# Kernel optimization log

Hardware: AMD Instinct MI355X
Metric: run time of the kernel (lower is better)

Reference implementation:

```python
import jax, jax.numpy as jnp
import numpy as np
from jax import lax

B, TIN, N, M, O, LM, TDEC = 64, 128, 256, 1024, 512, 2048, 64
LN_EPS = 1e-5


def setup_inputs() -> dict:
    key = jax.random.key(0)
    ks = jax.random.split(key, 32)
    s = 0.02
    p = lambda k, shape: (jax.random.normal(k, shape, jnp.float32) * s)
    z = lambda n: jnp.zeros((n,), jnp.float32)
    return {
        "X": jax.random.normal(ks[0], (B, TIN, N), jnp.float32),
        "Y0": jax.random.uniform(ks[1], (B, 1, O), jnp.float32),
        # encoder GRU, 2 layers (PyTorch layout: W_ih [3m,in], W_hh [3m,m])
        "enc_Wih0": p(ks[2], (3 * M, N)), "enc_Whh0": p(ks[3], (3 * M, M)),
        "enc_bih0": z(3 * M), "enc_bhh0": z(3 * M),
        "enc_Wih1": p(ks[4], (3 * M, M)), "enc_Whh1": p(ks[5], (3 * M, M)),
        "enc_bih1": z(3 * M), "enc_bhh1": z(3 * M),
        # decoder GRU, 2 layers (layer0 input dim = O)
        "dec_Wih0": p(ks[6], (3 * M, O)), "dec_Whh0": p(ks[7], (3 * M, M)),
        "dec_bih0": z(3 * M), "dec_bhh0": z(3 * M),
        "dec_Wih1": p(ks[8], (3 * M, M)), "dec_Whh1": p(ks[9], (3 * M, M)),
        "dec_bih1": z(3 * M), "dec_bhh1": z(3 * M),
        # decoder head
        "fc1_w": p(ks[10], (LM, M)), "fc1_b": z(LM),
        "ln_g": jnp.ones((LM,), jnp.float32), "ln_b": z(LM),
        "fc2_w": p(ks[11], (O, LM)), "fc2_b": z(O),
    }


def _gru_step(h, x, Wih, Whh, bih, bhh):
    # PyTorch GRU cell: gates ordered (r, z, n)
    gi = x @ Wih.T + bih          # [B, 3m]
    gh = h @ Whh.T + bhh          # [B, 3m]
    i_r, i_z, i_n = jnp.split(gi, 3, axis=-1)
    h_r, h_z, h_n = jnp.split(gh, 3, axis=-1)
    r = jax.nn.sigmoid(i_r + h_r)
    zg = jax.nn.sigmoid(i_z + h_z)
    n = jnp.tanh(i_n + r * h_n)
    return (1.0 - zg) * n + zg * h


def reference(X, Y0,
              enc_Wih0, enc_Whh0, enc_bih0, enc_bhh0,
              enc_Wih1, enc_Whh1, enc_bih1, enc_bhh1,
              dec_Wih0, dec_Whh0, dec_bih0, dec_bhh0,
              dec_Wih1, dec_Whh1, dec_bih1, dec_bhh1,
              fc1_w, fc1_b, ln_g, ln_b, fc2_w, fc2_b):
    batch = X.shape[0]
    # ---- encoder: 2-layer GRU over time ----
    seq = jnp.swapaxes(X, 0, 1)  # [T, B, n]
    enc_layers = [(enc_Wih0, enc_Whh0, enc_bih0, enc_bhh0),
                  (enc_Wih1, enc_Whh1, enc_bih1, enc_bhh1)]
    h_final = []
    for (Wih, Whh, bih, bhh) in enc_layers:
        def f(h, x, Wih=Wih, Whh=Whh, bih=bih, bhh=bhh):
            hn = _gru_step(h, x, Wih, Whh, bih, bhh)
            return hn, hn
        hT, seq = lax.scan(f, jnp.zeros((batch, M), X.dtype), seq)
        h_final.append(hT)

    dec0 = (dec_Wih0, dec_Whh0, dec_bih0, dec_bhh0)
    dec1 = (dec_Wih1, dec_Whh1, dec_bih1, dec_bhh1)
    y_init = Y0[:, 0, :]  # [B, o]

    def step(carry, _):
        h0, h1, y = carry
        h0n = _gru_step(h0, y, *dec0)
        h1n = _gru_step(h1, h0n, *dec1)
        z = h1n @ fc1_w.T + fc1_b                      # [B, l_m]
        mu = jnp.mean(z, axis=-1, keepdims=True)
        var = jnp.var(z, axis=-1, keepdims=True)
        z = (z - mu) * lax.rsqrt(var + LN_EPS) * ln_g + ln_b
        z = jax.nn.gelu(z, approximate=False)
        out = z @ fc2_w.T + fc2_b                      # [B, o]
        yn = jax.nn.softmax(out, axis=-1)
        return (h0n, h1n, yn), out

    _, outs = lax.scan(step, (h_final[0], h_final[1], y_init), None, length=TDEC)
    return jnp.swapaxes(outs, 0, 1)  # [B, TDEC, o]
```

## Files before the change

kernel.cpp:

```cpp
#include <hip/hip_runtime.h>
#include <math.h>

#define B 64
#define TIN 128
#define N_IN 256
#define M 1024
#define O_DIM 512
#define LM 2048
#define TDEC 64
#define M3 3072
#define CH 8
#define NB 256

typedef short bf16x8 __attribute__((ext_vector_type(8)));
typedef float floatx4 __attribute__((ext_vector_type(4)));
typedef unsigned long long u64_t;

__device__ __forceinline__ unsigned short f2bf(float f) {
    unsigned int u = __float_as_uint(f);
    u += 0x7FFFu + ((u >> 16) & 1u);
    return (unsigned short)(u >> 16);
}
__device__ __forceinline__ float sigm(float x) { return 1.f / (1.f + expf(-x)); }

__device__ __forceinline__ float ald_f(const float* p) {
    return __hip_atomic_load((float*)p, __ATOMIC_RELAXED, __HIP_MEMORY_SCOPE_AGENT);
}
__device__ __forceinline__ void ast_f(float* p, float v) {
    __hip_atomic_store(p, v, __ATOMIC_RELAXED, __HIP_MEMORY_SCOPE_AGENT);
}
__device__ __forceinline__ void ast_u(unsigned* p, unsigned v) {
    __hip_atomic_store(p, v, __ATOMIC_RELAXED, __HIP_MEMORY_SCOPE_AGENT);
}
__device__ __forceinline__ bf16x8 ald_b8(const short* p) {
    u64_t lo = __hip_atomic_load((u64_t*)p, __ATOMIC_RELAXED, __HIP_MEMORY_SCOPE_AGENT);
    u64_t hi = __hip_atomic_load((u64_t*)(p + 4), __ATOMIC_RELAXED, __HIP_MEMORY_SCOPE_AGENT);
    union { u64_t q[2]; bf16x8 v; } u;
    u.q[0] = lo; u.q[1] = hi;
    return u.v;
}
__device__ __forceinline__ void ast_h_pair(short* addr_even, float hv) {
    unsigned short hb16 = f2bf(hv);
    int partner = __shfl_xor((int)hb16, 1, 64);
    if ((threadIdx.x & 1) == 0) {
        unsigned pair = (unsigned)hb16 | ((unsigned)(unsigned short)partner << 16);
        __hip_atomic_store((unsigned*)addr_even, pair,
                           __ATOMIC_RELAXED, __HIP_MEMORY_SCOPE_AGENT);
    }
}

__device__ __forceinline__ void gridbar(unsigned* flags, unsigned epoch, int bid) {
    __syncthreads();
    if (threadIdx.x == 0)
        __hip_atomic_store(&flags[(size_t)bid * 32], epoch, __ATOMIC_RELAXED,
                           __HIP_MEMORY_SCOPE_AGENT);
    unsigned g = 0;
    while (__hip_atomic_load(&flags[(size_t)threadIdx.x * 32],
                             __ATOMIC_RELAXED, __HIP_MEMORY_SCOPE_AGENT) < epoch) {
        __builtin_amdgcn_s_sleep(2);
        if (++g > (1u << 22)) break;
    }
    __syncthreads();
}

__global__ __launch_bounds__(256) void cast_bf(const float* __restrict__ in,
                                               short* __restrict__ out, int n) {
    int i = blockIdx.x * 256 + threadIdx.x;
    if (i < n) out[i] = (short)f2bf(in[i]);
}

__global__ __launch_bounds__(256) void transpose_X_bf(const float* __restrict__ X,
                                                      short* __restrict__ Xt) {
    int idx = blockIdx.x * 256 + threadIdx.x;
    int n = idx & (N_IN - 1);
    int b = (idx >> 8) & (B - 1);
    int t = idx >> 14;
    Xt[idx] = (short)f2bf(X[(b * TIN + t) * N_IN + n]);
}

struct EncArgs {
    const short* Xt;
    short* seqA;
    float* gi;
    const short* wih0; const short* whh0; const float* bih0; const float* bhh0;
    const short* wih1; const short* whh1; const float* bih1; const float* bhh1;
    float* h0f; float* h1f;
    short* h0b; short* h1b;
    unsigned* flags;
};

__global__ __launch_bounds__(256, 1) void enc_mega(EncArgs a) {
    __shared__ float lds[3][4][64][4];
    const int bid  = blockIdx.x;
    const int wave = threadIdx.x >> 6;
    const int lane = threadIdx.x & 63;
    const int lrow = lane & 15;
    const int ko8  = (lane >> 4) * 8;
    unsigned epoch = 0;

    for (int layer = 0; layer < 2; ++layer) {
        const short* Wih = layer ? a.wih1 : a.wih0;
        const short* Whh = layer ? a.whh1 : a.whh0;
        const float* bih = layer ? a.bih1 : a.bih0;
        const float* bhh = layer ? a.bhh1 : a.bhh0;
        const short* inseq = layer ? a.seqA : a.Xt;
        const int K = layer ? M : N_IN;
        float* hf = layer ? a.h1f : a.h0f;
        short* hb = layer ? a.h1b : a.h0b;

        for (int c = 0; c < TIN / CH; ++c) {
            {
                const short* A = inseq + (size_t)c * CH * B * K;
                int xcd = bid & 7;
                int l   = bid >> 3;
                int w4  = l * 4 + wave;
                for (int i = 0; i < 6; ++i) {
                    int gt   = w4 * 6 + i;
                    int colt = xcd * 24 + (gt % 24);
                    int rowt = gt / 24;
                    int r0 = rowt * 16;
                    int c0 = colt * 16;
                    const short* ap = A + (size_t)(r0 + lrow) * K + ko8;
                    const short* wp = Wih + (size_t)(c0 + lrow) * K + ko8;
                    floatx4 acc = {0.f, 0.f, 0.f, 0.f};
                    #pragma unroll 4
                    for (int k = 0; k < K; k += 32) {
                        bf16x8 av = *(const bf16x8*)(ap + k);
                        bf16x8 bv = *(const bf16x8*)(wp + k);
                        acc = __builtin_amdgcn_mfma_f32_16x16x32_bf16(av, bv, acc, 0, 0, 0);
                    }
                    int col = c0 + lrow;
                    float bv = bih[col];
                    int rb = r0 + (lane >> 4) * 4;
                    #pragma unroll
                    for (int q = 0; q < 4; q++)
                        ast_f(&a.gi[(size_t)(rb + q) * M3 + col], acc[q] + bv);
                }
            }
            gridbar(a.flags, ++epoch, bid);
            for (int tt = 0; tt < CH; ++tt) {
                int t = c * CH + tt;
                int pin = t & 1, pout = pin ^ 1;
                const short* h_in = hb + (size_t)pin * B * M;
                float* gi_t = a.gi + (size_t)tt * B * M3;
                int m0 = (bid & 63) * 16;
                int r0 = (bid >> 6) * 16;
                const int Kq = M >> 2;
                const short* ap = h_in + (size_t)(r0 + lrow) * M + wave * Kq + ko8;
                bf16x8 hreg[8];
                #pragma unroll
                for (int k = 0; k < 8; ++k) hreg[k] = ald_b8(ap + k * 32);
                const short* wr = Whh + (size_t)(m0 + lrow) * M + wave * Kq + ko8;
                const short* wz = wr + (size_t)M * M;
                const short* wn = wr + (size_t)2 * M * M;
                floatx4 ar = {0.f, 0.f, 0.f, 0.f};
                floatx4 az = {0.f, 0.f, 0.f, 0.f};
                floatx4 ah = {0.f, 0.f, 0.f, 0.f};
                #pragma unroll
                for (int k = 0; k < 8; ++k) {
                    ar = __builtin_amdgcn_mfma_f32_16x16x32_bf16(hreg[k], *(const bf16x8*)(wr + k * 32), ar, 0, 0, 0);
                    az = __builtin_amdgcn_mfma_f32_16x16x32_bf16(hreg[k], *(const bf16x8*)(wz + k * 32), az, 0, 0, 0);
                    ah = __builtin_amdgcn_mfma_f32_16x16x32_bf16(hreg[k], *(const bf16x8*)(wn + k * 32), ah, 0, 0, 0);
                }
                #pragma unroll
                for (int i = 0; i < 4; i++) {
                    lds[0][wave][lane][i] = ar[i];
                    lds[1][wave][lane][i] = az[i];
                    lds[2][wave][lane][i] = ah[i];
                }
                __syncthreads();
                int row = threadIdx.x >> 4, col = threadIdx.x & 15;
                int sl = (row >> 2) * 16 + col, rg = row & 3;
                float sr = lds[0][0][sl][rg] + lds[0][1][sl][rg] + lds[0][2][sl][rg] + lds[0][3][sl][rg];
                float sz = lds[1][0][sl][rg] + lds[1][1][sl][rg] + lds[1][2][sl][rg] + lds[1][3][sl][rg];
                float sn = lds[2][0][sl][rg] + lds[2][1][sl][rg] + lds[2][2][sl][rg] + lds[2][3][sl][rg];
                int b = r0 + row, m = m0 + col;
                float gr = ald_f(&gi_t[(size_t)b * M3 + m]);
                float gz = ald_f(&gi_t[(size_t)b * M3 + M + m]);
                float gn = ald_f(&gi_t[(size_t)b * M3 + 2 * M + m]);
                float r = sigm(gr + sr + bhh[m]);
                float z = sigm(gz + sz + bhh[M + m]);
                float n = tanhf(gn + r * (sn + bhh[2 * M + m]));
                size_t hi = (size_t)b * M + m;
                float hv = (1.f - z) * n + z * hf[hi];
                hf[hi] = hv;
                if (layer == 0) a.seqA[(size_t)t * B * M + hi] = (short)f2bf(hv);
                ast_h_pair(hb + (size_t)pout * B * M + (size_t)b * M + (m & ~1),
                           hv);
                gridbar(a.flags, ++epoch, bid);
            }
        }
        if (layer == 0) {
            __builtin_amdgcn_fence(__ATOMIC_RELEASE, "agent");
            gridbar(a.flags, ++epoch, bid);
            __builtin_amdgcn_fence(__ATOMIC_ACQUIRE, "agent");
        }
    }
}

struct DecArgs {
    const short* yb;
    const short* wih0; const short* whh0; const float* bih0; const float* bhh0;
    const short* wih1; const short* whh1; const float* bih1; const float* bhh1;
    const short* wfc1; const float* fc1b;
    const float* lng; const float* lnb;
    const short* wfc2; const float* fc2b;
    float* h0f; float* h1f;
    short* h0b; short* h1b;
    float* zb;
    short* zbb;
    float* part;
    float* out;
    unsigned* flags;
};

__global__ __launch_bounds__(256, 1) void dec_mega(DecArgs a) {
    __shared__ short xs[16 * O_DIM];
    __shared__ float lds[4][4][64][4];
    __shared__ float redD[2];
    const int bid  = blockIdx.x;
    const int wave = threadIdx.x >> 6;
    const int lane = threadIdx.x & 63;
    const int lrow = lane & 15;
    const int ko8  = (lane >> 4) * 8;
    const int ldl  = TDEC * O_DIM;
    unsigned epoch = 0;

    for (int t = 0; t < TDEC; ++t) {
        int pin = t & 1, pout = pin ^ 1;
        int m0 = (bid & 63) * 16;
        int r0 = (bid >> 6) * 16;
        {
            const int KqH = M >> 2;
            const short* apH = a.h0b + (size_t)pin * B * M + (size_t)(r0 + lrow) * M + wave * KqH + ko8;
            bf16x8 hreg[8];
            #pragma unroll
            for (int k = 0; k < 8; ++k) hreg[k] = ald_b8(apH + k * 32);

            int rr = wave * 4 + (lane >> 4);
            int cl = lane & 15;
            if (t > 0) {
                const float* rowp = a.out + (size_t)(r0 + rr) * ldl
                                  + (size_t)(t - 1) * O_DIM + cl * 32;
                float v[32];
                float mx = -3.4e38f;
                #pragma unroll
                for (int j = 0; j < 32; j++) { v[j] = ald_f(rowp + j); mx = fmaxf(mx, v[j]); }
                #pragma unroll
                for (int off = 1; off < 16; off <<= 1) mx = fmaxf(mx, __shfl_xor(mx, off, 16));
                float s = 0.f;
                #pragma unroll
                for (int j = 0; j < 32; j++) { v[j] = __expf(v[j] - mx); s += v[j]; }
                #pragma unroll
                for (int off = 1; off < 16; off <<= 1) s += __shfl_xor(s, off, 16);
                float inv = 1.f / s;
                #pragma unroll
                for (int j = 0; j < 32; j += 2) {
                    unsigned int pk = (unsigned int)f2bf(v[j] * inv)
                                    | ((unsigned int)f2bf(v[j + 1] * inv) << 16);
                    int byte = ((rr * O_DIM + cl * 32 + j) * 2) ^ ((rr & 7) << 4);
                    *(unsigned int*)((char*)xs + byte) = pk;
                }
            } else {
                const short* rowp = a.yb + (size_t)(r0 + rr) * O_DIM + cl * 32;
                #pragma unroll
                for (int j = 0; j < 32; j += 2) {
                    unsigned int pk = (unsigned int)(unsigned short)rowp[j]
                                    | ((unsigned int)(unsigned short)rowp[j + 1] << 16);
                    int byte = ((rr * O_DIM + cl * 32 + j) * 2) ^ ((rr & 7) << 4);
                    *(unsigned int*)((char*)xs + byte) = pk;
                }
            }
            __syncthreads();
            const int KqI = O_DIM >> 2;
            const short* wrI = a.wih0 + (size_t)(m0 + lrow) * O_DIM + wave * KqI + ko8;
            const short* wzI = wrI + (size_t)M * O_DIM;
            const short* wnI = wrI + (size_t)2 * M * O_DIM;
            const short* wrH = a.whh0 + (size_t)(m0 + lrow) * M + wave * KqH + ko8;
            const short* wzH = wrH + (size_t)M * M;
            const short* wnH = wrH + (size_t)2 * M * M;
            floatx4 ar = {0.f, 0.f, 0.f, 0.f};
            floatx4 az = {0.f, 0.f, 0.f, 0.f};
            floatx4 ai = {0.f, 0.f, 0.f, 0.f};
            floatx4 ah = {0.f, 0.f, 0.f, 0.f};
            #pragma unroll
            for (int k = 0; k < KqI; k += 32) {
                int abyte = ((lrow * O_DIM + wave * KqI + ko8 + k) * 2) ^ ((lrow & 7) << 4);
                bf16x8 av = *(const bf16x8*)((const char*)xs + abyte);
                ar = __builtin_amdgcn_mfma_f32_16x16x32_bf16(av, *(const bf16x8*)(wrI + k), ar, 0, 0, 0);
                az = __builtin_amdgcn_mfma_f32_16x16x32_bf16(av, *(const bf16x8*)(wzI + k), az, 0, 0, 0);
                ai = __builtin_amdgcn_mfma_f32_16x16x32_bf16(av, *(const bf16x8*)(wnI + k), ai, 0, 0, 0);
            }
            #pragma unroll
            for (int k = 0; k < 8; ++k) {
                ar = __builtin_amdgcn_mfma_f32_16x16x32_bf16(hreg[k], *(const bf16x8*)(wrH + k * 32), ar, 0, 0, 0);
                az = __builtin_amdgcn_mfma_f32_16x16x32_bf16(hreg[k], *(const bf16x8*)(wzH + k * 32), az, 0, 0, 0);
                ah = __builtin_amdgcn_mfma_f32_16x16x32_bf16(hreg[k], *(const bf16x8*)(wnH + k * 32), ah, 0, 0, 0);
            }
            #pragma unroll
            for (int i = 0; i < 4; i++) {
                lds[0][wave][lane][i] = ar[i];
                lds[1][wave][lane][i] = az[i];
                lds[2][wave][lane][i] = ai[i];
                lds[3][wave][lane][i] = ah[i];
            }
            __syncthreads();
            int row = threadIdx.x >> 4, col = threadIdx.x & 15;
            int sl = (row >> 2) * 16 + col, rg = row & 3;
            float sr = lds[0][0][sl][rg] + lds[0][1][sl][rg] + lds[0][2][sl][rg] + lds[0][3][sl][rg];
            float sz = lds[1][0][sl][rg] + lds[1][1][sl][rg] + lds[1][2][sl][rg] + lds[1][3][sl][rg];
            float si = lds[2][0][sl][rg] + lds[2][1][sl][rg] + lds[2][2][sl][rg] + lds[2][3][sl][rg];
            float sh = lds[3][0][sl][rg] + lds[3][1][sl][rg] + lds[3][2][sl][rg] + lds[3][3][sl][rg];
            int b = r0 + row, m = m0 + col;
            float r = sigm(sr + a.bih0[m] + a.bhh0[m]);
            float z = sigm(sz + a.bih0[M + m] + a.bhh0[M + m]);
            float n = tanhf(si + a.bih0[2 * M + m] + r * (sh + a.bhh0[2 * M + m]));
            size_t hi = (size_t)b * M + m;
            float hv = (1.f - z) * n + z * a.h0f[hi];
            a.h0f[hi] = hv;
            ast_h_pair(a.h0b + (size_t)pout * B * M + (size_t)b * M + (m & ~1), hv);
        }
        gridbar(a.flags, ++epoch, bid);
        {
            const int Kq = M >> 2;
            const short* apI = a.h0b + (size_t)pout * B * M + (size_t)(r0 + lrow) * M + wave * Kq + ko8;
            const short* apH = a.h1b + (size_t)pin * B * M + (size_t)(r0 + lrow) * M + wave * Kq + ko8;
            bf16x8 ireg[8], hreg[8];
            #pragma unroll
            for (int k = 0; k < 8; ++k) ireg[k] = ald_b8(apI + k * 32);
            #pragma unroll
            for (int k = 0; k < 8; ++k) hreg[k] = ald_b8(apH + k * 32);
            const short* wrI = a.wih1 + (size_t)(m0 + lrow) * M + wave * Kq + ko8;
            const short* wzI = wrI + (size_t)M * M;
            const short* wnI = wrI + (size_t)2 * M * M;
            const short* wrH = a.whh1 + (size_t)(m0 + lrow) * M + wave * Kq + ko8;
            const short* wzH = wrH + (size_t)M * M;
            const short* wnH = wrH + (size_t)2 * M * M;
            floatx4 ar = {0.f, 0.f, 0.f, 0.f};
            floatx4 az = {0.f, 0.f, 0.f, 0.f};
            floatx4 ai = {0.f, 0.f, 0.f, 0.f};
            floatx4 ah = {0.f, 0.f, 0.f, 0.f};
            #pragma unroll
            for (int k = 0; k < 8; ++k) {
                ar = __builtin_amdgcn_mfma_f32_16x16x32_bf16(ireg[k], *(const bf16x8*)(wrI + k * 32), ar, 0, 0, 0);
                az = __builtin_amdgcn_mfma_f32_16x16x32_bf16(ireg[k], *(const bf16x8*)(wzI + k * 32), az, 0, 0, 0);
                ai = __builtin_amdgcn_mfma_f32_16x16x32_bf16(ireg[k], *(const bf16x8*)(wnI + k * 32), ai, 0, 0, 0);
            }
            #pragma unroll
            for (int k = 0; k < 8; ++k) {
                ar = __builtin_amdgcn_mfma_f32_16x16x32_bf16(hreg[k], *(const bf16x8*)(wrH + k * 32), ar, 0, 0, 0);
                az = __builtin_amdgcn_mfma_f32_16x16x32_bf16(hreg[k], *(const bf16x8*)(wzH + k * 32), az, 0, 0, 0);
                ah = __builtin_amdgcn_mfma_f32_16x16x32_bf16(hreg[k], *(const bf16x8*)(wnH + k * 32), ah, 0, 0, 0);
            }
            #pragma unroll
            for (int i = 0; i < 4; i++) {
                lds[0][wave][lane][i] = ar[i];
                lds[1][wave][lane][i] = az[i];
                lds[2][wave][lane][i] = ai[i];
                lds[3][wave][lane][i] = ah[i];
            }
            __syncthreads();
            int row = threadIdx.x >> 4, col = threadIdx.x & 15;
            int sl = (row >> 2) * 16 + col, rg = row & 3;
            float sr = lds[0][0][sl][rg] + lds[0][1][sl][rg] + lds[0][2][sl][rg] + lds[0][3][sl][rg];
            float sz = lds[1][0][sl][rg] + lds[1][1][sl][rg] + lds[1][2][sl][rg] + lds[1][3][sl][rg];
            float si = lds[2][0][sl][rg] + lds[2][1][sl][rg] + lds[2][2][sl][rg] + lds[2][3][sl][rg];
            float sh = lds[3][0][sl][rg] + lds[3][1][sl][rg] + lds[3][2][sl][rg] + lds[3][3][sl][rg];
            int b = r0 + row, m = m0 + col;
            float r = sigm(sr + a.bih1[m] + a.bhh1[m]);
            float z = sigm(sz + a.bih1[M + m] + a.bhh1[M + m]);
            float n = tanhf(si + a.bih1[2 * M + m] + r * (sh + a.bhh1[2 * M + m]));
            size_t hi = (size_t)b * M + m;
            float hv = (1.f - z) * n + z * a.h1f[hi];
            a.h1f[hi] = hv;
            ast_h_pair(a.h1b + (size_t)pout * B * M + (size_t)b * M + (m & ~1), hv);
        }
        gridbar(a.flags, ++epoch, bid);
        {
            const int Kq = M >> 2;
            const short* ap = a.h1b + (size_t)pout * B * M + (size_t)(r0 + lrow) * M + wave * Kq + ko8;
            bf16x8 hreg[8];
            #pragma unroll
            for (int k = 0; k < 8; ++k) hreg[k] = ald_b8(ap + k * 32);
            const short* wp0 = a.wfc1 + (size_t)((0 * 64 + (bid & 63)) * 16 + lrow) * M + wave * Kq + ko8;
            const short* wp1 = a.wfc1 + (size_t)((1 * 64 + (bid & 63)) * 16 + lrow) * M + wave * Kq + ko8;
            floatx4 acc0 = {0.f, 0.f, 0.f, 0.f};
            floatx4 acc1 = {0.f, 0.f, 0.f, 0.f};
            #pragma unroll
            for (int k = 0; k < 8; ++k) {
                acc0 = __builtin_amdgcn_mfma_f32_16x16x32_bf16(hreg[k], *(const bf16x8*)(wp0 + k * 32), acc0, 0, 0, 0);
                acc1 = __builtin_amdgcn_mfma_f32_16x16x32_bf16(hreg[k], *(const bf16x8*)(wp1 + k * 32), acc1, 0, 0, 0);
            }
            #pragma unroll
            for (int i = 0; i < 4; i++) {
                lds[0][wave][lane][i] = acc0[i];
                lds[1][wave][lane][i] = acc1[i];
            }
            __syncthreads();
            int row = threadIdx.x >> 4, col = threadIdx.x & 15;
            int sl = (row >> 2) * 16 + col, rg = row & 3;
            float svt = 0.f, sqt = 0.f;
            #pragma unroll
            for (int j = 0; j < 2; ++j) {
                int c0 = (j * 64 + (bid & 63)) * 16;
                float s = lds[j][0][sl][rg] + lds[j][1][sl][rg]
                        + lds[j][2][sl][rg] + lds[j][3][sl][rg];
                float val = s + a.fc1b[c0 + col];
                ast_f(&a.zb[(size_t)(r0 + row) * LM + c0 + col], val);
                svt += val;
                sqt += val * val;
            }
            #pragma unroll
            for (int off = 1; off < 16; off <<= 1) {
                svt += __shfl_xor(svt, off, 16);
                sqt += __shfl_xor(sqt, off, 16);
            }
            if ((threadIdx.x & 15) == 0) {
                size_t base = (size_t)t * 2 * 64 * 64;
                ast_f(&a.part[base + (size_t)(r0 + row) * 64 + (bid & 63)], svt);
                ast_f(&a.part[base + 64 * 64 + (size_t)(r0 + row) * 64 + (bid & 63)], sqt);
            }
        }
        gridbar(a.flags, ++epoch, bid);
        {
            int rowg = bid >> 2;
            if (wave < 2) {
                size_t base = (size_t)t * 2 * 64 * 64 + (size_t)wave * 64 * 64;
                float v = ald_f(&a.part[base + (size_t)rowg * 64 + lane]);
                #pragma unroll
                for (int off = 32; off > 0; off >>= 1) v += __shfl_down(v, off, 64);
                if (lane == 0) redD[wave] = v;
            }
            __syncthreads();
            float mu = redD[0] * (1.f / LM);
            float var = redD[1] * (1.f / LM) - mu * mu;
            float inv = rsqrtf(var + 1e-5f);
            int e0 = (bid * 256 + threadIdx.x) * 2;
            float ge[2];
            #pragma unroll
            for (int j = 0; j < 2; j++) {
                int e = e0 + j;
                int cc = e & (LM - 1);
                float zn = (ald_f(&a.zb[e]) - mu) * inv * a.lng[cc] + a.lnb[cc];
                ge[j] = 0.5f * zn * (1.f + erff(zn * 0.70710678118654752f));
            }
            unsigned pk = (unsigned)f2bf(ge[0]) | ((unsigned)f2bf(ge[1]) << 16);
            ast_u((unsigned*)(a.zbb + e0), pk);
        }
        gridbar(a.flags, ++epoch, bid);
        if (bid < 128) {
            int c0 = (bid & 31) * 16;
            int r0e = (bid >> 5) * 16;
            const int Kq = LM >> 2;
            const short* ap = a.zbb + (size_t)(r0e + lrow) * LM + wave * Kq + ko8;
            const short* wpp = a.wfc2 + (size_t)(c0 + lrow) * LM + wave * Kq + ko8;
            floatx4 acc = {0.f, 0.f, 0.f, 0.f};
            #pragma unroll
            for (int half = 0; half < 2; ++half) {
                bf16x8 zreg[8];
                #pragma unroll
                for (int k = 0; k < 8; ++k)
                    zreg[k] = ald_b8(ap + half * 256 + k * 32);
                #pragma unroll
                for (int k = 0; k < 8; ++k)
                    acc = __builtin_amdgcn_mfma_f32_16x16x32_bf16(
                        zreg[k], *(const bf16x8*)(wpp + half * 256 + k * 32), acc, 0, 0, 0);
            }
            #pragma unroll
            for (int i = 0; i < 4; i++) lds[0][wave][lane][i] = acc[i];
            __syncthreads();
            int row = threadIdx.x >> 4, col = threadIdx.x & 15;
            int sl = (row >> 2) * 16 + col, rg = row & 3;
            float s = lds[0][0][sl][rg] + lds[0][1][sl][rg]
                    + lds[0][2][sl][rg] + lds[0][3][sl][rg];
            ast_f(&a.out[(size_t)(r0e + row) * ldl + (size_t)t * O_DIM + c0 + col],
                  s + a.fc2b[c0 + col]);
        }
        gridbar(a.flags, ++epoch, bid);
    }
}

extern "C" void kernel_launch(void* const* d_in, const int* in_sizes, int n_in,
                              void* d_out, int out_size, void* d_ws, size_t ws_size,
                              hipStream_t stream) {
    const float* X        = (const float*)d_in[0];
    const float* Y0       = (const float*)d_in[1];
    const float* enc_Wih0 = (const float*)d_in[2];
    const float* enc_Whh0 = (const float*)d_in[3];
    const float* enc_bih0 = (const float*)d_in[4];
    const float* enc_bhh0 = (const float*)d_in[5];
    const float* enc_Wih1 = (const float*)d_in[6];
    const float* enc_Whh1 = (const float*)d_in[7];
    const float* enc_bih1 = (const float*)d_in[8];
    const float* enc_bhh1 = (const float*)d_in[9];
    const float* dec_Wih0 = (const float*)d_in[10];
    const float* dec_Whh0 = (const float*)d_in[11];
    const float* dec_bih0 = (const float*)d_in[12];
    const float* dec_bhh0 = (const float*)d_in[13];
    const float* dec_Wih1 = (const float*)d_in[14];
    const float* dec_Whh1 = (const float*)d_in[15];
    const float* dec_bih1 = (const float*)d_in[16];
    const float* dec_bhh1 = (const float*)d_in[17];
    const float* fc1_w    = (const float*)d_in[18];
    const float* fc1_b    = (const float*)d_in[19];
    const float* ln_g     = (const float*)d_in[20];
    const float* ln_b     = (const float*)d_in[21];
    const float* fc2_w    = (const float*)d_in[22];
    const float* fc2_b    = (const float*)d_in[23];
    float* out = (float*)d_out;

    char* p = (char*)d_ws;
    auto carve = [&](size_t bytes) {
        void* r = p;
        p += (bytes + 255) & ~(size_t)255;
        return r;
    };
    short* Xt    = (short*)carve((size_t)TIN * B * N_IN * 2);
    short* seqA  = (short*)carve((size_t)TIN * B * M * 2);
    float* gi_ch = (float*)carve((size_t)CH * B * M3 * 4);
    short* we_ih0 = (short*)carve((size_t)M3 * N_IN * 2);
    short* we_hh0 = (short*)carve((size_t)M3 * M * 2);
    short* we_ih1 = (short*)carve((size_t)M3 * M * 2);
    short* we_hh1 = (short*)carve((size_t)M3 * M * 2);
    short* wd_ih0 = (short*)carve((size_t)M3 * O_DIM * 2);
    short* wd_hh0 = (short*)carve((size_t)M3 * M * 2);
    short* wd_ih1 = (short*)carve((size_t)M3 * M * 2);
    short* wd_hh1 = (short*)carve((size_t)M3 * M * 2);
    short* wfc1   = (short*)carve((size_t)LM * M * 2);
    short* wfc2   = (short*)carve((size_t)O_DIM * LM * 2);
    float* h0f = (float*)carve((size_t)B * M * 4);
    float* h1f = (float*)carve((size_t)B * M * 4);
    short* h0b = (short*)carve((size_t)2 * B * M * 2);
    short* h1b = (short*)carve((size_t)2 * B * M * 2);
    short* yb  = (short*)carve((size_t)B * O_DIM * 2);
    float* zb  = (float*)carve((size_t)B * LM * 4);
    short* zbb = (short*)carve((size_t)B * LM * 2);
    float* part = (float*)carve((size_t)TDEC * 2 * 64 * 64 * 4);
    unsigned* eflags = (unsigned*)carve((size_t)NB * 32 * 4);
    unsigned* dflags = (unsigned*)carve((size_t)NB * 32 * 4);

    auto cast = [&](const float* src, short* dst, int n) {
        cast_bf<<<(n + 255) / 256, 256, 0, stream>>>(src, dst, n);
    };
    cast(enc_Wih0, we_ih0, M3 * N_IN);
    cast(enc_Whh0, we_hh0, M3 * M);
    cast(enc_Wih1, we_ih1, M3 * M);
    cast(enc_Whh1, we_hh1, M3 * M);
    cast(dec_Wih0, wd_ih0, M3 * O_DIM);
    cast(dec_Whh0, wd_hh0, M3 * M);
    cast(dec_Wih1, wd_ih1, M3 * M);
    cast(dec_Whh1, wd_hh1, M3 * M);
    cast(fc1_w, wfc1, LM * M);
    cast(fc2_w, wfc2, O_DIM * LM);
    cast(Y0, yb, B * O_DIM);
    transpose_X_bf<<<(TIN * B * N_IN) / 256, 256, 0, stream>>>(X, Xt);

    hipMemsetAsync(h0f, 0, (size_t)B * M * 4, stream);
    hipMemsetAsync(h1f, 0, (size_t)B * M * 4, stream);
    hipMemsetAsync(h0b, 0, (size_t)B * M * 2, stream);
    hipMemsetAsync(h1b, 0, (size_t)B * M * 2, stream);
    hipMemsetAsync(eflags, 0, (size_t)NB * 32 * 4, stream);
    hipMemsetAsync(dflags, 0, (size_t)NB * 32 * 4, stream);

    EncArgs ea;
    ea.Xt = Xt; ea.seqA = seqA; ea.gi = gi_ch;
    ea.wih0 = we_ih0; ea.whh0 = we_hh0; ea.bih0 = enc_bih0; ea.bhh0 = enc_bhh0;
    ea.wih1 = we_ih1; ea.whh1 = we_hh1; ea.bih1 = enc_bih1; ea.bhh1 = enc_bhh1;
    ea.h0f = h0f; ea.h1f = h1f; ea.h0b = h0b; ea.h1b = h1b;
    ea.flags = eflags;
    enc_mega<<<dim3(NB), dim3(256), 0, stream>>>(ea);

    DecArgs da;
    da.yb = yb;
    da.wih0 = wd_ih0; da.whh0 = wd_hh0; da.bih0 = dec_bih0; da.bhh0 = dec_bhh0;
    da.wih1 = wd_ih1; da.whh1 = wd_hh1; da.bih1 = dec_bih1; da.bhh1 = dec_bhh1;
    da.wfc1 = wfc1; da.fc1b = fc1_b;
    da.lng = ln_g; da.lnb = ln_b;
    da.wfc2 = wfc2; da.fc2b = fc2_b;
    da.h0f = h0f; da.h1f = h1f; da.h0b = h0b; da.h1b = h1b;
    da.zb = zb; da.zbb = zbb; da.part = part; da.out = out;
    da.flags = dflags;
    dec_mega<<<dim3(NB), dim3(256), 0, stream>>>(da);
}
```

Before: 6.380 ms.

## Fuse encoder input projection into per-block LDS and fold LayerNorm+GELU into fc2

The encoder's input-gate projection is now computed by each block only for the rows and columns it later consumes. The results stay in LDS instead of a global gi buffer, which removes one grid barrier per chunk. In the decoder, the separate LayerNorm/GELU phase and its grid barrier are dropped. The fc2 blocks compute the row stats and apply normalisation plus GELU on the fly while building MFMA operands. The grid barrier poll is also changed so a single wave checks four flags per lane. In exchange, each block does redundant LN/GELU work, and the encoder loses the XCD-aware tiling of the input GEMM.

```diff
diff --git a/kernel.cpp b/kernel.cpp
--- a/kernel.cpp
+++ b/kernel.cpp
@@ -26,16 +26,23 @@
 __device__ __forceinline__ float ald_f(const float* p) {
     return __hip_atomic_load((float*)p, __ATOMIC_RELAXED, __HIP_MEMORY_SCOPE_AGENT);
 }
+__device__ __forceinline__ unsigned ald_u32(const unsigned* p) {
+    return __hip_atomic_load((unsigned*)p, __ATOMIC_RELAXED, __HIP_MEMORY_SCOPE_AGENT);
+}
 __device__ __forceinline__ void ast_f(float* p, float v) {
-    __hip_atomic_store(p, v, __ATOMIC_RELAXED, __HIP_MEMORY_SCOPE_AGENT);
-}
-__device__ __forceinline__ void ast_u(unsigned* p, unsigned v) {
     __hip_atomic_store(p, v, __ATOMIC_RELAXED, __HIP_MEMORY_SCOPE_AGENT);
 }
 __device__ __forceinline__ bf16x8 ald_b8(const short* p) {
     u64_t lo = __hip_atomic_load((u64_t*)p, __ATOMIC_RELAXED, __HIP_MEMORY_SCOPE_AGENT);
     u64_t hi = __hip_atomic_load((u64_t*)(p + 4), __ATOMIC_RELAXED, __HIP_MEMORY_SCOPE_AGENT);
     union { u64_t q[2]; bf16x8 v; } u;
+    u.q[0] = lo; u.q[1] = hi;
+    return u.v;
+}
+__device__ __forceinline__ floatx4 ald_f4(const float* p) {
+    u64_t lo = __hip_atomic_load((u64_t*)p, __ATOMIC_RELAXED, __HIP_MEMORY_SCOPE_AGENT);
+    u64_t hi = __hip_atomic_load((u64_t*)(p + 2), __ATOMIC_RELAXED, __HIP_MEMORY_SCOPE_AGENT);
+    union { u64_t q[2]; floatx4 v; } u;
     u.q[0] = lo; u.q[1] = hi;
     return u.v;
 }
@@ -54,11 +61,18 @@
     if (threadIdx.x == 0)
         __hip_atomic_store(&flags[(size_t)bid * 32], epoch, __ATOMIC_RELAXED,
                            __HIP_MEMORY_SCOPE_AGENT);
-    unsigned g = 0;
-    while (__hip_atomic_load(&flags[(size_t)threadIdx.x * 32],
-                             __ATOMIC_RELAXED, __HIP_MEMORY_SCOPE_AGENT) < epoch) {
-        __builtin_amdgcn_s_sleep(2);
-        if (++g > (1u << 22)) break;
+    if (threadIdx.x < 64) {
+        unsigned g = 0;
+        for (;;) {
+            unsigned a0 = ald_u32(&flags[(size_t)threadIdx.x * 32]);
+            unsigned a1 = ald_u32(&flags[(size_t)(threadIdx.x + 64) * 32]);
+            unsigned a2 = ald_u32(&flags[(size_t)(threadIdx.x + 128) * 32]);
+            unsigned a3 = ald_u32(&flags[(size_t)(threadIdx.x + 192) * 32]);
+            bool done = (a0 >= epoch) & (a1 >= epoch) & (a2 >= epoch) & (a3 >= epoch);
+            if (__all(done)) break;
+            if (++g > (1u << 22)) break;
+            __builtin_amdgcn_s_sleep(4);
+        }
     }
     __syncthreads();
 }
@@ -81,7 +95,6 @@
 struct EncArgs {
     const short* Xt;
     short* seqA;
-    float* gi;
     const short* wih0; const short* whh0; const float* bih0; const float* bhh0;
     const short* wih1; const short* whh1; const float* bih1; const float* bhh1;
     float* h0f; float* h1f;
@@ -91,11 +104,14 @@
 
 __global__ __launch_bounds__(256, 1) void enc_mega(EncArgs a) {
     __shared__ float lds[3][4][64][4];
+    __shared__ float gilds[CH][3][16][16];
     const int bid  = blockIdx.x;
     const int wave = threadIdx.x >> 6;
     const int lane = threadIdx.x & 63;
     const int lrow = lane & 15;
     const int ko8  = (lane >> 4) * 8;
+    const int m0 = (bid & 63) * 16;
+    const int r0 = (bid >> 6) * 16;
     unsigned epoch = 0;
 
     for (int layer = 0; layer < 2; ++layer) {
@@ -110,18 +126,12 @@
 
         for (int c = 0; c < TIN / CH; ++c) {
             {
-                const short* A = inseq + (size_t)c * CH * B * K;
-                int xcd = bid & 7;
-                int l   = bid >> 3;
-                int w4  = l * 4 + wave;
                 for (int i = 0; i < 6; ++i) {
-                    int gt   = w4 * 6 + i;
-                    int colt = xcd * 24 + (gt % 24);
-                    int rowt = gt / 24;
-                    int r0 = rowt * 16;
-                    int c0 = colt * 16;
-                    const short* ap = A + (size_t)(r0 + lrow) * K + ko8;
-                    const short* wp = Wih + (size_t)(c0 + lrow) * K + ko8;
+                    int idx = wave * 6 + i;
+                    int tt = idx / 3, g = idx % 3;
+                    const short* ap = inseq
+                        + ((size_t)(c * CH + tt) * B + r0 + lrow) * K + ko8;
+                    const short* wp = Wih + (size_t)(g * M + m0 + lrow) * K + ko8;
                     floatx4 acc = {0.f, 0.f, 0.f, 0.f};
                     #pragma unroll 4
                     for (int k = 0; k < K; k += 32) {
@@ -129,28 +139,22 @@
                         bf16x8 bv = *(const bf16x8*)(wp + k);
                         acc = __builtin_amdgcn_mfma_f32_16x16x32_bf16(av, bv, acc, 0, 0, 0);
                     }
-                    int col = c0 + lrow;
-                    float bv = bih[col];
-                    int rb = r0 + (lane >> 4) * 4;
+                    float bv = bih[g * M + m0 + lrow];
                     #pragma unroll
                     for (int q = 0; q < 4; q++)
-                        ast_f(&a.gi[(size_t)(rb + q) * M3 + col], acc[q] + bv);
+                        gilds[tt][g][(lane >> 4) * 4 + q][lrow] = acc[q] + bv;
                 }
-            }
-            gridbar(a.flags, ++epoch, bid);
+                __syncthreads();
+            }
             for (int tt = 0; tt < CH; ++tt) {
                 int t = c * CH + tt;
                 int pin = t & 1, pout = pin ^ 1;
-                const short* h_in = hb + (size_t)pin * B * M;
-                float* gi_t = a.gi + (size_t)tt * B * M3;
-                int m0 = (bid & 63) * 16;
-                int r0 = (bid >> 6) * 16;
-                const int Kq = M >> 2;
-                const short* ap = h_in + (size_t)(r0 + lrow) * M + wave * Kq + ko8;
+                const short* ap = hb + (size_t)pin * B * M
+                                + (size_t)(r0 + lrow) * M + wave * 256 + ko8;
                 bf16x8 hreg[8];
                 #pragma unroll
                 for (int k = 0; k < 8; ++k) hreg[k] = ald_b8(ap + k * 32);
-                const short* wr = Whh + (size_t)(m0 + lrow) * M + wave * Kq + ko8;
+                const short* wr = Whh + (size_t)(m0 + lrow) * M + wave * 256 + ko8;
                 const short* wz = wr + (size_t)M * M;
                 const short* wn = wr + (size_t)2 * M * M;
                 floatx4 ar = {0.f, 0.f, 0.f, 0.f};
@@ -175,9 +179,9 @@
                 float sz = lds[1][0][sl][rg] + lds[1][1][sl][rg] + lds[1][2][sl][rg] + lds[1][3][sl][rg];
                 float sn = lds[2][0][sl][rg] + lds[2][1][sl][rg] + lds[2][2][sl][rg] + lds[2][3][sl][rg];
                 int b = r0 + row, m = m0 + col;
-                float gr = ald_f(&gi_t[(size_t)b * M3 + m]);
-                float gz = ald_f(&gi_t[(size_t)b * M3 + M + m]);
-                float gn = ald_f(&gi_t[(size_t)b * M3 + 2 * M + m]);
+                float gr = gilds[tt][0][row][col];
+                float gz = gilds[tt][1][row][col];
+                float gn = gilds[tt][2][row][col];
                 float r = sigm(gr + sr + bhh[m]);
                 float z = sigm(gz + sz + bhh[M + m]);
                 float n = tanhf(gn + r * (sn + bhh[2 * M + m]));
@@ -208,7 +212,6 @@
     float* h0f; float* h1f;
     short* h0b; short* h1b;
     float* zb;
-    short* zbb;
     float* part;
     float* out;
     unsigned* flags;
@@ -217,7 +220,7 @@
 __global__ __launch_bounds__(256, 1) void dec_mega(DecArgs a) {
     __shared__ short xs[16 * O_DIM];
     __shared__ float lds[4][4][64][4];
-    __shared__ float redD[2];
+    __shared__ float statlds[16][2];
     const int bid  = blockIdx.x;
     const int wave = threadIdx.x >> 6;
     const int lane = threadIdx.x & 63;
@@ -231,8 +234,8 @@
         int m0 = (bid & 63) * 16;
         int r0 = (bid >> 6) * 16;
         {
-            const int KqH = M >> 2;
-            const short* apH = a.h0b + (size_t)pin * B * M + (size_t)(r0 + lrow) * M + wave * KqH + ko8;
+            const short* apH = a.h0b + (size_t)pin * B * M
+                             + (size_t)(r0 + lrow) * M + wave * 256 + ko8;
             bf16x8 hreg[8];
             #pragma unroll
             for (int k = 0; k < 8; ++k) hreg[k] = ald_b8(apH + k * 32);
@@ -276,7 +279,7 @@
             const short* wrI = a.wih0 + (size_t)(m0 + lrow) * O_DIM + wave * KqI + ko8;
             const short* wzI = wrI + (size_t)M * O_DIM;
             const short* wnI = wrI + (size_t)2 * M * O_DIM;
-            const short* wrH = a.whh0 + (size_t)(m0 + lrow) * M + wave * KqH + ko8;
+            const short* wrH = a.whh0 + (size_t)(m0 + lrow) * M + wave * 256 + ko8;
             const short* wzH = wrH + (size_t)M * M;
             const short* wnH = wrH + (size_t)2 * M * M;
             floatx4 ar = {0.f, 0.f, 0.f, 0.f};
@@ -322,18 +325,17 @@
         }
         gridbar(a.flags, ++epoch, bid);
         {
-            const int Kq = M >> 2;
-            const short* apI = a.h0b + (size_t)pout * B * M + (size_t)(r0 + lrow) * M + wave * Kq + ko8;
-            const short* apH = a.h1b + (size_t)pin * B * M + (size_t)(r0 + lrow) * M + wave * Kq + ko8;
+            const short* apI = a.h0b + (size_t)pout * B * M + (size_t)(r0 + lrow) * M + wave * 256 + ko8;
+            const short* apH = a.h1b + (size_t)pin * B * M + (size_t)(r0 + lrow) * M + wave * 256 + ko8;
             bf16x8 ireg[8], hreg[8];
             #pragma unroll
             for (int k = 0; k < 8; ++k) ireg[k] = ald_b8(apI + k * 32);
             #pragma unroll
             for (int k = 0; k < 8; ++k) hreg[k] = ald_b8(apH + k * 32);
-            const short* wrI = a.wih1 + (size_t)(m0 + lrow) * M + wave * Kq + ko8;
+            const short* wrI = a.wih1 + (size_t)(m0 + lrow) * M + wave * 256 + ko8;
             const short* wzI = wrI + (size_t)M * M;
             const short* wnI = wrI + (size_t)2 * M * M;
-            const short* wrH = a.whh1 + (size_t)(m0 + lrow) * M + wave * Kq + ko8;
+            const short* wrH = a.whh1 + (size_t)(m0 + lrow) * M + wave * 256 + ko8;
             const short* wzH = wrH + (size_t)M * M;
             const short* wnH = wrH + (size_t)2 * M * M;
             floatx4 ar = {0.f, 0.f, 0.f, 0.f};
@@ -377,13 +379,12 @@
         }
         gridbar(a.flags, ++epoch, bid);
         {
-            const int Kq = M >> 2;
-            const short* ap = a.h1b + (size_t)pout * B * M + (size_t)(r0 + lrow) * M + wave * Kq + ko8;
+            const short* ap = a.h1b + (size_t)pout * B * M + (size_t)(r0 + lrow) * M + wave * 256 + ko8;
             bf16x8 hreg[8];
             #pragma unroll
             for (int k = 0; k < 8; ++k) hreg[k] = ald_b8(ap + k * 32);
-            const short* wp0 = a.wfc1 + (size_t)((0 * 64 + (bid & 63)) * 16 + lrow) * M + wave * Kq + ko8;
-            const short* wp1 = a.wfc1 + (size_t)((1 * 64 + (bid & 63)) * 16 + lrow) * M + wave * Kq + ko8;
+            const short* wp0 = a.wfc1 + (size_t)((0 * 64 + (bid & 63)) * 16 + lrow) * M + wave * 256 + ko8;
+            const short* wp1 = a.wfc1 + (size_t)((1 * 64 + (bid & 63)) * 16 + lrow) * M + wave * 256 + ko8;
             floatx4 acc0 = {0.f, 0.f, 0.f, 0.f};
             floatx4 acc1 = {0.f, 0.f, 0.f, 0.f};
             #pragma unroll
@@ -422,49 +423,45 @@
             }
         }
         gridbar(a.flags, ++epoch, bid);
-        {
-            int rowg = bid >> 2;
-            if (wave < 2) {
-                size_t base = (size_t)t * 2 * 64 * 64 + (size_t)wave * 64 * 64;
-                float v = ald_f(&a.part[base + (size_t)rowg * 64 + lane]);
-                #pragma unroll
-                for (int off = 32; off > 0; off >>= 1) v += __shfl_down(v, off, 64);
-                if (lane == 0) redD[wave] = v;
-            }
-            __syncthreads();
-            float mu = redD[0] * (1.f / LM);
-            float var = redD[1] * (1.f / LM) - mu * mu;
-            float inv = rsqrtf(var + 1e-5f);
-            int e0 = (bid * 256 + threadIdx.x) * 2;
-            float ge[2];
-            #pragma unroll
-            for (int j = 0; j < 2; j++) {
-                int e = e0 + j;
-                int cc = e & (LM - 1);
-                float zn = (ald_f(&a.zb[e]) - mu) * inv * a.lng[cc] + a.lnb[cc];
-                ge[j] = 0.5f * zn * (1.f + erff(zn * 0.70710678118654752f));
-            }
-            unsigned pk = (unsigned)f2bf(ge[0]) | ((unsigned)f2bf(ge[1]) << 16);
-            ast_u((unsigned*)(a.zbb + e0), pk);
-        }
-        gridbar(a.flags, ++epoch, bid);
         if (bid < 128) {
             int c0 = (bid & 31) * 16;
             int r0e = (bid >> 5) * 16;
-            const int Kq = LM >> 2;
-            const short* ap = a.zbb + (size_t)(r0e + lrow) * LM + wave * Kq + ko8;
-            const short* wpp = a.wfc2 + (size_t)(c0 + lrow) * LM + wave * Kq + ko8;
+            int row16 = threadIdx.x >> 4, sub = threadIdx.x & 15;
+            size_t pb = (size_t)t * 2 * 64 * 64;
+            float S = 0.f, SS = 0.f;
+            #pragma unroll
+            for (int j = 0; j < 4; ++j) {
+                S  += ald_f(&a.part[pb + (size_t)(r0e + row16) * 64 + sub * 4 + j]);
+                SS += ald_f(&a.part[pb + 4096 + (size_t)(r0e + row16) * 64 + sub * 4 + j]);
+            }
+            #pragma unroll
+            for (int off = 1; off < 16; off <<= 1) {
+                S += __shfl_xor(S, off, 16);
+                SS += __shfl_xor(SS, off, 16);
+            }
+            if (sub == 0) { statlds[row16][0] = S; statlds[row16][1] = SS; }
+            __syncthreads();
+            float mu = statlds[lrow][0] * (1.f / LM);
+            float var = statlds[lrow][1] * (1.f / LM) - mu * mu;
+            float inv = rsqrtf(var + 1e-5f);
+            const float* zp = a.zb + (size_t)(r0e + lrow) * LM + wave * 512 + ko8;
+            const float* gp = a.lng + wave * 512 + ko8;
+            const float* bp = a.lnb + wave * 512 + ko8;
+            const short* wpp = a.wfc2 + (size_t)(c0 + lrow) * LM + wave * 512 + ko8;
             floatx4 acc = {0.f, 0.f, 0.f, 0.f};
-            #pragma unroll
-            for (int half = 0; half < 2; ++half) {
-                bf16x8 zreg[8];
-                #pragma unroll
-                for (int k = 0; k < 8; ++k)
-                    zreg[k] = ald_b8(ap + half * 256 + k * 32);
-                #pragma unroll
-                for (int k = 0; k < 8; ++k)
-                    acc = __builtin_amdgcn_mfma_f32_16x16x32_bf16(
-                        zreg[k], *(const bf16x8*)(wpp + half * 256 + k * 32), acc, 0, 0, 0);
+            for (int k = 0; k < 512; k += 32) {
+                floatx4 z0 = ald_f4(zp + k);
+                floatx4 z1 = ald_f4(zp + k + 4);
+                bf16x8 av;
+                #pragma unroll
+                for (int j = 0; j < 8; ++j) {
+                    float zv = (j < 4) ? z0[j] : z1[j - 4];
+                    float zn = (zv - mu) * inv * gp[k + j] + bp[k + j];
+                    float ge = 0.5f * zn * (1.f + erff(zn * 0.70710678118654752f));
+                    av[j] = (short)f2bf(ge);
+                }
+                acc = __builtin_amdgcn_mfma_f32_16x16x32_bf16(
+                    av, *(const bf16x8*)(wpp + k), acc, 0, 0, 0);
             }
             #pragma unroll
             for (int i = 0; i < 4; i++) lds[0][wave][lane][i] = acc[i];
@@ -517,7 +514,6 @@
     };
     short* Xt    = (short*)carve((size_t)TIN * B * N_IN * 2);
     short* seqA  = (short*)carve((size_t)TIN * B * M * 2);
-    float* gi_ch = (float*)carve((size_t)CH * B * M3 * 4);
     short* we_ih0 = (short*)carve((size_t)M3 * N_IN * 2);
     short* we_hh0 = (short*)carve((size_t)M3 * M * 2);
     short* we_ih1 = (short*)carve((size_t)M3 * M * 2);
@@ -534,7 +530,6 @@
     short* h1b = (short*)carve((size_t)2 * B * M * 2);
     short* yb  = (short*)carve((size_t)B * O_DIM * 2);
     float* zb  = (float*)carve((size_t)B * LM * 4);
-    short* zbb = (short*)carve((size_t)B * LM * 2);
     float* part = (float*)carve((size_t)TDEC * 2 * 64 * 64 * 4);
     unsigned* eflags = (unsigned*)carve((size_t)NB * 32 * 4);
     unsigned* dflags = (unsigned*)carve((size_t)NB * 32 * 4);
@@ -563,7 +558,7 @@
     hipMemsetAsync(dflags, 0, (size_t)NB * 32 * 4, stream);
 
     EncArgs ea;
-    ea.Xt = Xt; ea.seqA = seqA; ea.gi = gi_ch;
+    ea.Xt = Xt; ea.seqA = seqA;
     ea.wih0 = we_ih0; ea.whh0 = we_hh0; ea.bih0 = enc_bih0; ea.bhh0 = enc_bhh0;
     ea.wih1 = we_ih1; ea.whh1 = we_hh1; ea.bih1 = enc_bih1; ea.bhh1 = enc_bhh1;
     ea.h0f = h0f; ea.h1f = h1f; ea.h0b = h0b; ea.h1b = h1b;
@@ -578,7 +573,7 @@
     da.lng = ln_g; da.lnb = ln_b;
     da.wfc2 = wfc2; da.fc2b = fc2_b;
     da.h0f = h0f; da.h1f = h1f; da.h0b = h0b; da.h1b = h1b;
-    da.zb = zb; da.zbb = zbb; da.part = part; da.out = out;
+    da.zb = zb; da.part = part; da.out = out;
     da.flags = dflags;
     dec_mega<<<dim3(NB), dim3(256), 0, stream>>>(da);
 }
```

After: 7.329 ms. 14.9% more time.
